# Optimization experiments

Hardware: AMD Instinct MI355X
Metric: run time of the kernel (lower is better)

Reference implementation:

```python
import jax, jax.numpy as jnp
import numpy as np

D_MODEL = 1024
N_HEADS = 16
HEAD_DIM = 64
D_FF = 4096


def rmsnorm(x, w):
    eps = jnp.finfo(x.dtype).eps
    var = jnp.mean(jnp.square(x), axis=-1, keepdims=True)
    return x * jax.lax.rsqrt(var + eps) * w


def setup_inputs() -> dict:
    key = jax.random.key(0)
    ks = jax.random.split(key, 8)
    d, h, hd, dff = D_MODEL, N_HEADS, HEAD_DIM, D_FF
    s = 0.02
    return {
        "x": jax.random.normal(ks[0], (2, 2048, d), dtype=jnp.float32),
        "norm_w": jnp.ones((d,), dtype=jnp.float32),
        "Wq": jax.random.normal(ks[1], (d, h * hd), dtype=jnp.float32) * s,
        "Wk": jax.random.normal(ks[2], (d, h * hd), dtype=jnp.float32) * s,
        "Wv": jax.random.normal(ks[3], (d, h * hd), dtype=jnp.float32) * s,
        "Wo": jax.random.normal(ks[4], (h * hd, d), dtype=jnp.float32) * s,
        "W1": jax.random.normal(ks[5], (d, dff), dtype=jnp.float32) * s,
        "W2": jax.random.normal(ks[6], (dff, d), dtype=jnp.float32) * s,
    }


def reference(x, norm_w, Wq, Wk, Wv, Wo, W1, W2):
    B, T, d = x.shape
    h, hd = N_HEADS, HEAD_DIM
    scale = 1.0 / np.sqrt(hd)

    xn = rmsnorm(x, norm_w)

    # attention branch
    q = (xn @ Wq).reshape(B, T, h, hd).transpose(0, 2, 1, 3)  # [B,h,T,hd]
    k = (xn @ Wk).reshape(B, T, h, hd).transpose(0, 2, 1, 3)
    v = (xn @ Wv).reshape(B, T, h, hd).transpose(0, 2, 1, 3)
    attn = jnp.einsum("bhqd,bhkd->bhqk", q, k) * scale
    causal = jnp.tril(jnp.ones((T, T), dtype=bool))
    attn = jnp.where(causal, attn, -jnp.inf)
    attn = jax.nn.softmax(attn, axis=-1)
    out = jnp.einsum("bhqk,bhkd->bhqd", attn, v)
    out = out.transpose(0, 2, 1, 3).reshape(B, T, h * hd)
    attn_out = out @ Wo

    # FFN branch
    ffn_out = jax.nn.silu(xn @ W1) @ W2

    return x + attn_out + ffn_out
```

## Files before the change

### kernel.cpp

```cpp
#include <hip/hip_runtime.h>

#define DM   1024
#define DFF  4096
#define NH   16
#define HD   64
#define TT   2048
#define BT   4096
#define KC   5120

typedef unsigned short u16;
typedef unsigned int   u32;
typedef __attribute__((ext_vector_type(8))) short s16x8;
typedef __attribute__((ext_vector_type(4))) float f32x4;

__device__ __forceinline__ u16 f2bf(float f) {
  u32 u = __builtin_bit_cast(u32, f);
  u += 0x7fffu + ((u >> 16) & 1u);
  return (u16)(u >> 16);
}

__device__ __forceinline__ void gl2lds16(const void* g, void* l) {
  __builtin_amdgcn_global_load_lds((__attribute__((address_space(1))) void*)(g),
                                   (__attribute__((address_space(3))) void*)(l),
                                   16, 0, 0);
}

__global__ __launch_bounds__(256) void rmsnorm_k(const float* __restrict__ x,
                                                 const float* __restrict__ w,
                                                 u16* __restrict__ xn) {
  const int row = blockIdx.x;
  const int t = threadIdx.x;
  const float4 v = ((const float4*)(x + (size_t)row * DM))[t];
  float ss = v.x*v.x + v.y*v.y + v.z*v.z + v.w*v.w;
  #pragma unroll
  for (int off = 32; off; off >>= 1) ss += __shfl_xor(ss, off, 64);
  __shared__ float red[4];
  if ((t & 63) == 0) red[t >> 6] = ss;
  __syncthreads();
  const float tot = red[0] + red[1] + red[2] + red[3];
  const float r = __builtin_amdgcn_rsqf(tot * (1.0f / DM) + 1.1920929e-7f);
  const float4 wv = ((const float4*)w)[t];
  u16* o = xn + (size_t)row * DM + t * 4;
  o[0] = f2bf(v.x * r * wv.x);
  o[1] = f2bf(v.y * r * wv.y);
  o[2] = f2bf(v.z * r * wv.z);
  o[3] = f2bf(v.w * r * wv.w);
}

__global__ __launch_bounds__(256) void wtrans_k(const float* __restrict__ W,
                                                u16* __restrict__ Wt,
                                                int K, int N, int pitch, int koff) {
  __shared__ float tile[32][33];
  const int n0 = blockIdx.x * 32, k0 = blockIdx.y * 32;
  const int tx = threadIdx.x, ty = threadIdx.y;
  #pragma unroll
  for (int i = 0; i < 4; ++i)
    tile[ty + i*8][tx] = W[(size_t)(k0 + ty + i*8) * N + n0 + tx];
  __syncthreads();
  #pragma unroll
  for (int i = 0; i < 4; ++i)
    Wt[(size_t)(n0 + ty + i*8) * pitch + koff + k0 + tx] = f2bf(tile[tx][ty + i*8]);
}

__global__ __launch_bounds__(256, 2) void gemm_fused(const u16* __restrict__ A,
                                                     const u16* __restrict__ Bt,
                                                     u16* __restrict__ qkb,
                                                     u16* __restrict__ vtg,
                                                     u16* __restrict__ acat) {
  const int K = 1024;
  __shared__ u16 sA[128 * 32];
  __shared__ u16 sB[128 * 32];
  const int t = threadIdx.x;
  const int lane = t & 63, wave = t >> 6;
  const int quad = lane >> 4, l4 = lane & 15;
  const int wy = wave >> 1, wx = wave & 1;
  const size_t mBase = (size_t)blockIdx.y * 128;
  const size_t nBase = (size_t)blockIdx.x * 128;
  const int r  = t >> 2;
  const int c8 = (t & 3) * 8;
  const u16* Ag0 = A + (mBase + r) * K + c8;
  const u16* Ag1 = Ag0 + (size_t)64 * K;
  const u16* Bg0 = Bt + (nBase + r) * K + c8;
  const u16* Bg1 = Bg0 + (size_t)64 * K;
  char* sAb = (char*)sA + (wave << 10);
  char* sBb = (char*)sB + (wave << 10);

  f32x4 acc[4][4];
  #pragma unroll
  for (int i = 0; i < 4; ++i)
    #pragma unroll
    for (int j = 0; j < 4; ++j)
      acc[i][j] = (f32x4)0.0f;

  for (int k0 = 0; k0 < K; k0 += 32) {
    __syncthreads();
    gl2lds16(Ag0 + k0, sAb);
    gl2lds16(Ag1 + k0, sAb + 4096);
    gl2lds16(Bg0 + k0, sBb);
    gl2lds16(Bg1 + k0, sBb + 4096);
    __syncthreads();
    s16x8 af[4], bfr[4];
    #pragma unroll
    for (int i = 0; i < 4; ++i)
      af[i] = *(const s16x8*)&sA[(wy*64 + i*16 + l4) * 32 + quad*8];
    #pragma unroll
    for (int j = 0; j < 4; ++j)
      bfr[j] = *(const s16x8*)&sB[(wx*64 + j*16 + l4) * 32 + quad*8];
    #pragma unroll
    for (int i = 0; i < 4; ++i)
      #pragma unroll
      for (int j = 0; j < 4; ++j)
        acc[i][j] = __builtin_amdgcn_mfma_f32_16x16x32_bf16(af[i], bfr[j], acc[i][j], 0, 0, 0);
  }

  #pragma unroll
  for (int i = 0; i < 4; ++i) {
    const size_t row0 = mBase + wy*64 + i*16 + quad*4;
    #pragma unroll
    for (int j = 0; j < 4; ++j) {
      const int col = (int)nBase + wx*64 + j*16 + l4;
      if (nBase < 1024) {
        #pragma unroll
        for (int rg = 0; rg < 4; ++rg)
          qkb[(row0 + rg) * 2048 + col] = f2bf(acc[i][j][rg] * 0.18033688011f);
      } else if (nBase < 2048) {
        #pragma unroll
        for (int rg = 0; rg < 4; ++rg)
          qkb[(row0 + rg) * 2048 + col] = f2bf(acc[i][j][rg]);
      } else if (nBase < 3072) {
        const int cv = col - 2048, hh = cv >> 6, dd = cv & 63;
        const int bb = (int)(row0 >> 11), t0 = (int)(row0 & 2047);
        ushort4 pk;
        pk.x = f2bf(acc[i][j][0]); pk.y = f2bf(acc[i][j][1]);
        pk.z = f2bf(acc[i][j][2]); pk.w = f2bf(acc[i][j][3]);
        *(ushort4*)(vtg + ((size_t)((bb*16 + hh)*64 + dd)) * 2048 + t0) = pk;
      } else {
        #pragma unroll
        for (int rg = 0; rg < 4; ++rg) {
          float v = acc[i][j][rg];
          v = v / (1.0f + __expf(-v));
          acat[(row0 + rg) * (size_t)KC + 1024 + (col - 3072)] = f2bf(v);
        }
      }
    }
  }
}

__global__ __launch_bounds__(512) void gemm_final(const u16* __restrict__ A,
                                                  const u16* __restrict__ Bt,
                                                  const float* __restrict__ x,
                                                  float* __restrict__ out) {
  __shared__ u16 sA[128 * 32];
  __shared__ u16 sB[128 * 32];
  const int t = threadIdx.x;
  const int lane = t & 63, wave = t >> 6;
  const int quad = lane >> 4, l4 = lane & 15;
  const int wy = wave >> 2, wx = wave & 3;
  const size_t mBase = (size_t)blockIdx.y * 128;
  const size_t nBase = (size_t)blockIdx.x * 128;
  const int r  = t >> 2;
  const int c8 = (t & 3) * 8;
  const u16* Ag = A  + (mBase + r) * KC + c8;
  const u16* Bg = Bt + (nBase + r) * KC + c8;
  char* sAb = (char*)sA + (wave << 10);
  char* sBb = (char*)sB + (wave << 10);

  f32x4 acc[4][2];
  #pragma unroll
  for (int i = 0; i < 4; ++i)
    #pragma unroll
    for (int j = 0; j < 2; ++j)
      acc[i][j] = (f32x4)0.0f;

  for (int k0 = 0; k0 < KC; k0 += 32) {
    __syncthreads();
    gl2lds16(Ag + k0, sAb);
    gl2lds16(Bg + k0, sBb);
    __syncthreads();
    s16x8 af[4], bfr[2];
    #pragma unroll
    for (int i = 0; i < 4; ++i)
      af[i] = *(const s16x8*)&sA[(wy*64 + i*16 + l4) * 32 + quad*8];
    #pragma unroll
    for (int j = 0; j < 2; ++j)
      bfr[j] = *(const s16x8*)&sB[(wx*32 + j*16 + l4) * 32 + quad*8];
    #pragma unroll
    for (int i = 0; i < 4; ++i)
      #pragma unroll
      for (int j = 0; j < 2; ++j)
        acc[i][j] = __builtin_amdgcn_mfma_f32_16x16x32_bf16(af[i], bfr[j], acc[i][j], 0, 0, 0);
  }

  #pragma unroll
  for (int i = 0; i < 4; ++i) {
    const size_t row0 = mBase + wy*64 + i*16 + quad*4;
    #pragma unroll
    for (int j = 0; j < 2; ++j) {
      const int col = (int)nBase + wx*32 + j*16 + l4;
      #pragma unroll
      for (int rg = 0; rg < 4; ++rg) {
        const size_t idx = (row0 + rg) * (size_t)DM + col;
        out[idx] = x[idx] + acc[i][j][rg];
      }
    }
  }
}

__global__ __launch_bounds__(128) void attn_k(const u16* __restrict__ qk,
                                              const u16* __restrict__ vtg,
                                              u16* __restrict__ acat) {
  const int bh = blockIdx.x, b = bh >> 4, h = bh & 15;
  const int qt = 63 - blockIdx.y;
  const int qw = qt * 32;
  const int wave = threadIdx.x >> 6, lane = threadIdx.x & 63;
  const int quad = lane >> 4, l4 = lane & 15;
  const u16* Qp = qk + (size_t)b * TT * 2048 + h * HD;
  const u16* Kp = Qp + 1024;
  const u16* Vp = vtg + (size_t)bh * 64 * 2048;

  __shared__ u16 Pb[2][32][72];
  __shared__ float Ob[32][68];
  __shared__ float Lb[32];

  s16x8 qf[2][2];
  #pragma unroll
  for (int mi = 0; mi < 2; ++mi)
    #pragma unroll
    for (int kf = 0; kf < 2; ++kf)
      qf[mi][kf] = *(const s16x8*)(Qp + (size_t)(qw + mi*16 + l4) * 2048 + kf*32 + quad*8);

  const s16x8 ones = {0x3F80,0x3F80,0x3F80,0x3F80,0x3F80,0x3F80,0x3F80,0x3F80};

  f32x4 o[2][4];
  f32x4 lacc[2];
  #pragma unroll
  for (int mi = 0; mi < 2; ++mi) {
    lacc[mi] = (f32x4)0.0f;
    #pragma unroll
    for (int ni = 0; ni < 4; ++ni) o[mi][ni] = (f32x4)0.0f;
  }

  const int n   = (qt + 2) >> 1;
  const int n0  = (n + 1) >> 1;
  const int kt0 = wave ? n0 : 0;
  const int kt1 = wave ? n : n0;

  for (int kt = kt0; kt < kt1; ++kt) {
    const int k0 = kt * 64;

    f32x4 st[4][2];
    #pragma unroll
    for (int nj = 0; nj < 4; ++nj) {
      const u16* kr = Kp + (size_t)(k0 + nj*16 + l4) * 2048 + quad*8;
      const s16x8 kf0 = *(const s16x8*)kr;
      const s16x8 kf1 = *(const s16x8*)(kr + 32);
      #pragma unroll
      for (int mi = 0; mi < 2; ++mi) {
        f32x4 a = (f32x4)0.0f;
        a = __builtin_amdgcn_mfma_f32_16x16x32_bf16(kf0, qf[mi][0], a, 0, 0, 0);
        a = __builtin_amdgcn_mfma_f32_16x16x32_bf16(kf1, qf[mi][1], a, 0, 0, 0);
        st[nj][mi] = a;
      }
    }

    s16x8 vb[2][4];
    #pragma unroll
    for (int kf2 = 0; kf2 < 2; ++kf2)
      #pragma unroll
      for (int ni = 0; ni < 4; ++ni)
        vb[kf2][ni] = *(const s16x8*)(Vp + (size_t)(ni*16 + l4) * 2048 + k0 + kf2*32 + quad*8);

    if (k0 + 63 > qw) {
      #pragma unroll
      for (int nj = 0; nj < 4; ++nj)
        #pragma unroll
        for (int mi = 0; mi < 2; ++mi)
          #pragma unroll
          for (int rg = 0; rg < 4; ++rg) {
            const int key = k0 + nj*16 + quad*4 + rg;
            const int q   = qw + mi*16 + l4;
            if (key > q) st[nj][mi][rg] = -1e30f;
          }
    }

    #pragma unroll
    for (int nj = 0; nj < 4; ++nj)
      #pragma unroll
      for (int mi = 0; mi < 2; ++mi) {
        float p0 = __builtin_amdgcn_exp2f(st[nj][mi][0]);
        float p1 = __builtin_amdgcn_exp2f(st[nj][mi][1]);
        float p2 = __builtin_amdgcn_exp2f(st[nj][mi][2]);
        float p3 = __builtin_amdgcn_exp2f(st[nj][mi][3]);
        uint2 w;
        w.x = __builtin_amdgcn_perm(__builtin_bit_cast(u32, p1),
                                    __builtin_bit_cast(u32, p0), 0x07060302u);
        w.y = __builtin_amdgcn_perm(__builtin_bit_cast(u32, p3),
                                    __builtin_bit_cast(u32, p2), 0x07060302u);
        *(uint2*)&Pb[wave][mi*16 + l4][nj*16 + quad*4] = w;
      }

    #pragma unroll
    for (int kf2 = 0; kf2 < 2; ++kf2) {
      s16x8 pa[2];
      #pragma unroll
      for (int mi = 0; mi < 2; ++mi)
        pa[mi] = *(const s16x8*)&Pb[wave][mi*16 + l4][kf2*32 + quad*8];
      #pragma unroll
      for (int mi = 0; mi < 2; ++mi) {
        lacc[mi] = __builtin_amdgcn_mfma_f32_16x16x32_bf16(pa[mi], ones, lacc[mi], 0, 0, 0);
        #pragma unroll
        for (int ni = 0; ni < 4; ++ni)
          o[mi][ni] = __builtin_amdgcn_mfma_f32_16x16x32_bf16(pa[mi], vb[kf2][ni], o[mi][ni], 0, 0, 0);
      }
    }
  }

  if (wave == 1) {
    #pragma unroll
    for (int mi = 0; mi < 2; ++mi)
      #pragma unroll
      for (int rg = 0; rg < 4; ++rg) {
        const int row = mi*16 + quad*4 + rg;
        #pragma unroll
        for (int ni = 0; ni < 4; ++ni) Ob[row][ni*16 + l4] = o[mi][ni][rg];
        if (l4 == 0) Lb[row] = lacc[mi][rg];
      }
  }
  __syncthreads();
  if (wave == 0) {
    #pragma unroll
    for (int mi = 0; mi < 2; ++mi)
      #pragma unroll
      for (int rg = 0; rg < 4; ++rg) {
        const int row = mi*16 + quad*4 + rg;
        const float inv = 1.0f / (lacc[mi][rg] + Lb[row]);
        #pragma unroll
        for (int ni = 0; ni < 4; ++ni)
          Pb[0][row][ni*16 + l4] = f2bf((o[mi][ni][rg] + Ob[row][ni*16 + l4]) * inv);
      }
    #pragma unroll
    for (int it = 0; it < 4; ++it) {
      const int row = it*8 + (lane >> 3);
      const int c0  = (lane & 7) * 8;
      const s16x8 pk = *(const s16x8*)&Pb[0][row][c0];
      *(s16x8*)(acat + ((size_t)b * TT + qw + row) * KC + h*HD + c0) = pk;
    }
  }
}

extern "C" void kernel_launch(void* const* d_in, const int* in_sizes, int n_in,
                              void* d_out, int out_size, void* d_ws, size_t ws_size,
                              hipStream_t stream) {
  (void)in_sizes; (void)n_in; (void)out_size; (void)ws_size;
  const float* x  = (const float*)d_in[0];
  const float* nw = (const float*)d_in[1];
  const float* Wq = (const float*)d_in[2];
  const float* Wk = (const float*)d_in[3];
  const float* Wv = (const float*)d_in[4];
  const float* Wo = (const float*)d_in[5];
  const float* W1 = (const float*)d_in[6];
  const float* W2 = (const float*)d_in[7];

  char* ws = (char*)d_ws;
  u16*   xn      = (u16*)(ws);
  u16*   wqkv1_t = (u16*)(ws + ((size_t)8  << 20));
  u16*   bcat    = (u16*)(ws + ((size_t)22 << 20));
  u16*   qkb     = (u16*)(ws + ((size_t)32 << 20));
  u16*   vtg     = (u16*)(ws + ((size_t)48 << 20));
  u16*   acat    = (u16*)(ws + ((size_t)56 << 20));
  float* dout    = (float*)d_out;

  rmsnorm_k<<<BT, 256, 0, stream>>>(x, nw, xn);
  const dim3 tb(32, 8);
  wtrans_k<<<dim3(32, 32),  tb, 0, stream>>>(Wq, wqkv1_t,                      1024, 1024, 1024, 0);
  wtrans_k<<<dim3(32, 32),  tb, 0, stream>>>(Wk, wqkv1_t + (size_t)1024*1024,  1024, 1024, 1024, 0);
  wtrans_k<<<dim3(32, 32),  tb, 0, stream>>>(Wv, wqkv1_t + (size_t)2048*1024,  1024, 1024, 1024, 0);
  wtrans_k<<<dim3(128, 32), tb, 0, stream>>>(W1, wqkv1_t + (size_t)3072*1024,  1024, 4096, 1024, 0);
  wtrans_k<<<dim3(32, 32),  tb, 0, stream>>>(Wo, bcat,                         1024, 1024, 5120, 0);
  wtrans_k<<<dim3(32, 128), tb, 0, stream>>>(W2, bcat,                         4096, 1024, 5120, 1024);

  gemm_fused<<<dim3(56, 32), 256, 0, stream>>>(xn, wqkv1_t, qkb, vtg, acat);
  attn_k<<<dim3(32, 64), 128, 0, stream>>>(qkb, vtg, acat);
  gemm_final<<<dim3(8, 32), 512, 0, stream>>>(acat, bcat, x, dout);
}
```

Before: 377.2 us.

## Double-buffer LDS tiles in both GEMM kernels to overlap loads with MFMA

Both GEMM kernels now keep two LDS buffers and prefetch the next K tile with global_load_lds while the current tile feeds the MFMAs. This cuts each iteration to a single barrier, so global latency can be hidden behind compute. In the final GEMM each stage also grows to 64 in K, with two sub-steps per barrier, which halves the number of synchronisations. The cost is more LDS per block (doubled in gemm_fused, quadrupled in gemm_final), which may lower occupancy.

```diff
diff --git a/kernel.cpp b/kernel.cpp
--- a/kernel.cpp
+++ b/kernel.cpp
@@ -68,8 +68,8 @@
                                                      u16* __restrict__ vtg,
                                                      u16* __restrict__ acat) {
   const int K = 1024;
-  __shared__ u16 sA[128 * 32];
-  __shared__ u16 sB[128 * 32];
+  __shared__ u16 sA[2 * 128 * 32];
+  __shared__ u16 sB[2 * 128 * 32];
   const int t = threadIdx.x;
   const int lane = t & 63, wave = t >> 6;
   const int quad = lane >> 4, l4 = lane & 15;
@@ -92,20 +92,27 @@
     for (int j = 0; j < 4; ++j)
       acc[i][j] = (f32x4)0.0f;
 
-  for (int k0 = 0; k0 < K; k0 += 32) {
+  auto issue = [&](int bf, int k0) {
+    gl2lds16(Ag0 + k0, sAb + bf*8192);
+    gl2lds16(Ag1 + k0, sAb + bf*8192 + 4096);
+    gl2lds16(Bg0 + k0, sBb + bf*8192);
+    gl2lds16(Bg1 + k0, sBb + bf*8192 + 4096);
+  };
+
+  issue(0, 0);
+  for (int kt = 0; kt < 32; ++kt) {
+    const int bf = kt & 1;
     __syncthreads();
-    gl2lds16(Ag0 + k0, sAb);
-    gl2lds16(Ag1 + k0, sAb + 4096);
-    gl2lds16(Bg0 + k0, sBb);
-    gl2lds16(Bg1 + k0, sBb + 4096);
-    __syncthreads();
+    if (kt + 1 < 32) issue(bf ^ 1, (kt + 1) * 32);
+    const u16* pA = sA + bf * 4096;
+    const u16* pB = sB + bf * 4096;
     s16x8 af[4], bfr[4];
     #pragma unroll
     for (int i = 0; i < 4; ++i)
-      af[i] = *(const s16x8*)&sA[(wy*64 + i*16 + l4) * 32 + quad*8];
+      af[i] = *(const s16x8*)&pA[(wy*64 + i*16 + l4) * 32 + quad*8];
     #pragma unroll
     for (int j = 0; j < 4; ++j)
-      bfr[j] = *(const s16x8*)&sB[(wx*64 + j*16 + l4) * 32 + quad*8];
+      bfr[j] = *(const s16x8*)&pB[(wx*64 + j*16 + l4) * 32 + quad*8];
     #pragma unroll
     for (int i = 0; i < 4; ++i)
       #pragma unroll
@@ -150,8 +157,8 @@
                                                   const u16* __restrict__ Bt,
                                                   const float* __restrict__ x,
                                                   float* __restrict__ out) {
-  __shared__ u16 sA[128 * 32];
-  __shared__ u16 sB[128 * 32];
+  __shared__ u16 sA[2 * 2 * 128 * 32];
+  __shared__ u16 sB[2 * 2 * 128 * 32];
   const int t = threadIdx.x;
   const int lane = t & 63, wave = t >> 6;
   const int quad = lane >> 4, l4 = lane & 15;
@@ -162,8 +169,8 @@
   const int c8 = (t & 3) * 8;
   const u16* Ag = A  + (mBase + r) * KC + c8;
   const u16* Bg = Bt + (nBase + r) * KC + c8;
-  char* sAb = (char*)sA + (wave << 10);
-  char* sBb = (char*)sB + (wave << 10);
+  char* sAw = (char*)sA + (wave << 10);
+  char* sBw = (char*)sB + (wave << 10);
 
   f32x4 acc[4][2];
   #pragma unroll
@@ -172,23 +179,36 @@
     for (int j = 0; j < 2; ++j)
       acc[i][j] = (f32x4)0.0f;
 
-  for (int k0 = 0; k0 < KC; k0 += 32) {
+  auto issue = [&](int bf, int k0) {
+    gl2lds16(Ag + k0,      sAw + bf*16384);
+    gl2lds16(Ag + k0 + 32, sAw + bf*16384 + 8192);
+    gl2lds16(Bg + k0,      sBw + bf*16384);
+    gl2lds16(Bg + k0 + 32, sBw + bf*16384 + 8192);
+  };
+
+  issue(0, 0);
+  const int NIT = KC / 64;
+  for (int kt = 0; kt < NIT; ++kt) {
+    const int bf = kt & 1;
     __syncthreads();
-    gl2lds16(Ag + k0, sAb);
-    gl2lds16(Bg + k0, sBb);
-    __syncthreads();
-    s16x8 af[4], bfr[2];
-    #pragma unroll
-    for (int i = 0; i < 4; ++i)
-      af[i] = *(const s16x8*)&sA[(wy*64 + i*16 + l4) * 32 + quad*8];
-    #pragma unroll
-    for (int j = 0; j < 2; ++j)
-      bfr[j] = *(const s16x8*)&sB[(wx*32 + j*16 + l4) * 32 + quad*8];
-    #pragma unroll
-    for (int i = 0; i < 4; ++i)
+    if (kt + 1 < NIT) issue(bf ^ 1, (kt + 1) * 64);
+    #pragma unroll
+    for (int s = 0; s < 2; ++s) {
+      const u16* pA = sA + (bf*2 + s) * 4096;
+      const u16* pB = sB + (bf*2 + s) * 4096;
+      s16x8 af[4], bfr[2];
+      #pragma unroll
+      for (int i = 0; i < 4; ++i)
+        af[i] = *(const s16x8*)&pA[(wy*64 + i*16 + l4) * 32 + quad*8];
       #pragma unroll
       for (int j = 0; j < 2; ++j)
-        acc[i][j] = __builtin_amdgcn_mfma_f32_16x16x32_bf16(af[i], bfr[j], acc[i][j], 0, 0, 0);
+        bfr[j] = *(const s16x8*)&pB[(wx*32 + j*16 + l4) * 32 + quad*8];
+      #pragma unroll
+      for (int i = 0; i < 4; ++i)
+        #pragma unroll
+        for (int j = 0; j < 2; ++j)
+          acc[i][j] = __builtin_amdgcn_mfma_f32_16x16x32_bf16(af[i], bfr[j], acc[i][j], 0, 0, 0);
+    }
   }
 
   #pragma unroll
```

Result: no change. 373.9 us (-0.9%).
